# Kernel tuning notes

Measured on AMD Instinct MI355X. Metric: run time of the kernel, lower is better.

The kernel has to match this reference:

```python
import jax, jax.numpy as jnp
import numpy as np

STRIDE = 1
PADDING = 1

def setup_inputs() -> dict:
    key = jax.random.key(0)
    k1, k2 = jax.random.split(key)
    x = jax.random.normal(k1, (16, 64, 224, 224), dtype=jnp.float32)
    weight = jax.random.normal(k2, (64, 64, 3, 3), dtype=jnp.float32)
    return {"x": x, "weight": weight}

def reference(x, weight):
    # Module's per-tap shift-and-add loop is exactly cross-correlation conv2d:
    # weight indexed [out, in, kh, kw] with ZeroPad2d(padding) and given stride.
    return jax.lax.conv_general_dilated(
        x, weight,
        window_strides=(STRIDE, STRIDE),
        padding=((PADDING, PADDING), (PADDING, PADDING)),
        dimension_numbers=("NCHW", "OIHW", "NCHW"),
    )
```

## Files before the change

### kernel.cpp

```cpp
#include <hip/hip_runtime.h>


#define HH 224
#define WW 224
#define CHW (HH * WW)
#define PLANE 4352
#define NSLOT 18

typedef short bf16x8 __attribute__((ext_vector_type(8)));
typedef float f32x16 __attribute__((ext_vector_type(16)));

__device__ __forceinline__ unsigned short f2bf(float f) {
    union { float f; unsigned int u; } v; v.f = f;
    unsigned int u = v.u;
    return (unsigned short)((u + 0x7fffu + ((u >> 16) & 1u)) >> 16);
}

#define SGB  __builtin_amdgcn_sched_group_barrier
#define MFMA __builtin_amdgcn_mfma_f32_32x32x16_bf16

__device__ __forceinline__ void block_fence_lds() {
    asm volatile("s_waitcnt lgkmcnt(0)" ::: "memory");
    __builtin_amdgcn_s_barrier();
    __builtin_amdgcn_sched_barrier(0);
}

__global__ void wprep_kernel(const float* __restrict__ wgt, unsigned short* __restrict__ wb) {
    const int i = blockIdx.x * 256 + threadIdx.x;
    if (i >= 36864) return;
    const int j   = i & 7;
    const int oc  = (i >> 3) & 63;
    const int g   = (i >> 9) & 1;
    const int ks  = i >> 10;
    const int tap = ks >> 2;
    const int c   = (ks & 3) * 16 + g * 8 + j;
    wb[i] = f2bf(wgt[(oc * 64 + c) * 9 + tap]);
}

#define MMA_CQ(dw, cq, WFU) do {                                              \
    const int off_ = (((cq) * 32 + g16) ^ swz_);                              \
    const bf16x8 B0 = *(const bf16x8*)(ldsB + sl0 + wb_ + off_);              \
    const bf16x8 B1 = *(const bf16x8*)(ldsB + sl1 + wb_ + off_);              \
    const bf16x8 B2 = *(const bf16x8*)(ldsB + sl2 + wb_ + off_);              \
    const bf16x8 B3 = *(const bf16x8*)(ldsB + sl3 + wb_ + off_);              \
    const bf16x8 B4 = *(const bf16x8*)(ldsB + sl4 + wb_ + off_);              \
    const bf16x8 B5 = *(const bf16x8*)(ldsB + sl5 + wb_ + off_);              \
    a0 = MFMA(wfrag[(dw)*4 + (cq)], B0, a0, 0, 0, 0);                         \
    a1 = MFMA(wfrag[(dw)*4 + (cq)], B1, a1, 0, 0, 0);                         \
    a2 = MFMA(wfrag[(dw)*4 + (cq)], B2, a2, 0, 0, 0);                         \
    a3 = MFMA(wfrag[(dw)*4 + (cq)], B3, a3, 0, 0, 0);                         \
    a0 = MFMA(wfrag[12 + (dw)*4 + (cq)], B1, a0, 0, 0, 0);                    \
    a1 = MFMA(wfrag[12 + (dw)*4 + (cq)], B2, a1, 0, 0, 0);                    \
    a2 = MFMA(wfrag[12 + (dw)*4 + (cq)], B3, a2, 0, 0, 0);                    \
    a3 = MFMA(wfrag[12 + (dw)*4 + (cq)], B4, a3, 0, 0, 0);                    \
    a0 = MFMA(WFU, B2, a0, 0, 0, 0);                                          \
    a1 = MFMA(WFU, B3, a1, 0, 0, 0);                                          \
    a2 = MFMA(WFU, B4, a2, 0, 0, 0);                                          \
    a3 = MFMA(WFU, B5, a3, 0, 0, 0);                                          \
    SGB(0x100, 6, 0); SGB(0x008, 12, 0);                                      \
} while (0)

#define SECTION(dw, cqp, WFU0, WFU1, WFLD0, WFLD1, ldw, lcqp) do {            \
    WFLD0 = *(const bf16x8*)(wlane + ((6 + (ldw))*4 + 2*(lcqp)    ) * 1024);  \
    WFLD1 = *(const bf16x8*)(wlane + ((6 + (ldw))*4 + 2*(lcqp) + 1) * 1024);  \
    const int wl_  = s + (dw);                                                \
    const int swz_ = (wl_ & 7) << 4;                                          \
    const int wb_  = wl_ * 128;                                               \
    MMA_CQ(dw, 2*(cqp),     WFU0);                                            \
    MMA_CQ(dw, 2*(cqp) + 1, WFU1);                                            \
} while (0)

#define STI(k) do { if (st) {                                                 \
    const int r_ = h + 9 + (k);                                               \
    const bool ok_ = (r_ < HH);                                               \
    _Pragma("unroll")                                                         \
    for (int j = 0; j < 8; ++j) pv[j] = ok_ ? pxm[j*CHW + r_*WW] : 0.f;       \
    if (tid >= 240) {                                                         \
        const bool okh_ = ok_ && hokw;                                        \
        _Pragma("unroll")                                                     \
        for (int j = 0; j < 8; ++j) hv[j] = okh_ ? pxh[j*CHW + r_*WW] : 0.f;  \
    } } } while (0)

#define STW(k) do { if (st) {                                                 \
    int sw_ = slw + (k); if (sw_ >= NSLOT) sw_ -= NSLOT;                      \
    bf16x8 f_;                                                                \
    _Pragma("unroll")                                                         \
    for (int j = 0; j < 8; ++j) f_[j] = (short)f2bf(pv[j]);                   \
    *(bf16x8*)(ldsB + sw_ * PLANE + lom) = f_;                                \
    if (tid >= 240) {                                                         \
        bf16x8 fh_;                                                           \
        _Pragma("unroll")                                                     \
        for (int j = 0; j < 8; ++j) fh_[j] = (short)f2bf(hv[j]);              \
        *(bf16x8*)(ldsB + sw_ * PLANE + loh) = fh_;                           \
    } } } while (0)

__global__ __launch_bounds__(256, 2)
void conv3x3_mfma(const float* __restrict__ x, const unsigned short* __restrict__ wb,
                  float* __restrict__ out) {
    __shared__ __align__(16) unsigned short lds[NSLOT * 34 * 64];
    char* ldsB = (char*)lds;

    const int tid  = threadIdx.x;
    const int lane = tid & 63;
    const int wv   = tid >> 6;
    const int och  = wv & 1;
    const int rg4  = wv >> 1;
    const int s    = lane & 31;
    const int g    = lane >> 5;
    const int g16  = g * 16;

    const int bid = blockIdx.x;
    const int n   = bid / 28;
    const int rem = bid % 28;
    const int ws  = rem / 4;
    const int hc  = rem % 4;
    const int wbase = ws * 32;
    const int h0    = hc * 56;

    const unsigned short* wlane = wb + g * 512 + (och * 32 + s) * 8;
    bf16x8 wfrag[24];
#pragma unroll
    for (int ks = 0; ks < 24; ++ks)
        wfrag[ks] = *(const bf16x8*)(wlane + ks * 1024);
    bf16x8 wfA0 = *(const bf16x8*)(wlane + 24 * 1024);
    bf16x8 wfA1 = *(const bf16x8*)(wlane + 25 * 1024);
    bf16x8 wfB0 = {}, wfB1 = {};

    for (int p = tid; p < 10 * 272; p += 256) {
        const int rrel = p / 272;
        const int q  = p % 272;
        const int c8 = q / 34;
        const int wl = q % 34;
        const int r  = h0 - 1 + rrel;
        const int gw = wbase - 1 + wl;
        bf16x8 f = {};
        if (r >= 0 && r < HH && gw >= 0 && gw < WW) {
            const float* px = x + (n * 64 + c8 * 8) * CHW + r * WW + gw;
#pragma unroll
            for (int j = 0; j < 8; ++j) f[j] = (short)f2bf(px[j * CHW]);
        }
        *(bf16x8*)(ldsB + ((r + NSLOT) % NSLOT) * PLANE + wl * 128
                   + ((c8 * 16) ^ ((wl & 7) << 4))) = f;
    }

    const int c8m = tid >> 5;
    const int wlm = 1 + (tid & 31);
    const float* pxm = x + (n * 64 + c8m * 8) * CHW + (wbase + (tid & 31));
    const int lom = wlm * 128 + ((c8m * 16) ^ ((wlm & 7) << 4));
    const int c8h = lane & 7;
    const int wlh = ((lane >> 3) & 1) * 33;
    const int gwh = wbase - 1 + wlh;
    const bool hokw = (gwh >= 0 && gwh < WW);
    const float* pxh = x + (n * 64 + c8h * 8) * CHW + gwh;
    const int loh = wlh * 128 + ((c8h * 16) ^ ((wlh & 7) << 4));

    block_fence_lds();

#pragma unroll 1
    for (int it = 0; it < 7; ++it) {
        const int h  = h0 + 8 * it;
        const int hb = h + 4 * rg4;
        const bool st = (it < 6);
        const int slw = (h + 9) % NSLOT;

        int t_ = (hb - 1 + NSLOT) % NSLOT;
        const int sl0 = t_ * PLANE; t_ = (t_ + 1 == NSLOT) ? 0 : t_ + 1;
        const int sl1 = t_ * PLANE; t_ = (t_ + 1 == NSLOT) ? 0 : t_ + 1;
        const int sl2 = t_ * PLANE; t_ = (t_ + 1 == NSLOT) ? 0 : t_ + 1;
        const int sl3 = t_ * PLANE; t_ = (t_ + 1 == NSLOT) ? 0 : t_ + 1;
        const int sl4 = t_ * PLANE; t_ = (t_ + 1 == NSLOT) ? 0 : t_ + 1;
        const int sl5 = t_ * PLANE;

        float pv[8], hv[8];
        f32x16 a0 = {}, a1 = {}, a2 = {}, a3 = {};

        STI(0); SECTION(0, 0, wfA0, wfA1, wfB0, wfB1, 0, 1); STW(0);
        STI(1); SECTION(0, 1, wfB0, wfB1, wfA0, wfA1, 1, 0); STW(1);
        STI(2); SECTION(1, 0, wfA0, wfA1, wfB0, wfB1, 1, 1); STW(2);
        STI(3); SECTION(1, 1, wfB0, wfB1, wfA0, wfA1, 2, 0); STW(3);
        STI(4); SECTION(2, 0, wfA0, wfA1, wfB0, wfB1, 2, 1); STW(4);
        STI(5); SECTION(2, 1, wfB0, wfB1, wfA0, wfA1, 0, 0); STW(5);

        float* po = out + (n * 64 + och * 32 + 4 * g) * CHW + hb * WW + wbase + s;
        STI(6);
#pragma unroll
        for (int rg = 0; rg < 16; ++rg) {
            const int o_ = ((rg & 3) + 8 * (rg >> 2)) * CHW;
            po[o_]      = a0[rg];
            po[o_ + WW] = a1[rg];
        }
        STW(6); STI(7);
#pragma unroll
        for (int rg = 0; rg < 16; ++rg) {
            const int o_ = ((rg & 3) + 8 * (rg >> 2)) * CHW;
            po[o_ + 2 * WW] = a2[rg];
            po[o_ + 3 * WW] = a3[rg];
        }
        STW(7);

        block_fence_lds();
    }
}

extern "C" void kernel_launch(void* const* d_in, const int* in_sizes, int n_in,
                              void* d_out, int out_size, void* d_ws, size_t ws_size,
                              hipStream_t stream) {
    const float* x   = (const float*)d_in[0];
    const float* wgt = (const float*)d_in[1];
    float* out       = (float*)d_out;
    unsigned short* wbuf = (unsigned short*)d_ws;

    wprep_kernel<<<dim3(144), dim3(256), 0, stream>>>(wgt, wbuf);
    conv3x3_mfma<<<dim3(448), dim3(256), 0, stream>>>(x, wbuf, out);
}
```

Before: 177.5 us.

## Halve per-block row tile, shrink LDS ring, raise occupancy to three blocks

Each block now covers 28 rows instead of 56, with each wave computing 2 output rows instead of 4. The grid doubles to 896 blocks and the LDS ring shrinks from 18 to 10 slots. Only 12 weight fragments stay resident and the rest stream through a three-deep rotation, cutting VGPR and LDS use so that launch bounds can ask for 3 blocks per CU. The cost is a larger halo overhead per block (6 loaded rows for 4 computed) and fewer MFMAs per barrier, which may reduce reuse and latency hiding.

```diff
diff --git a/kernel.cpp b/kernel.cpp
--- a/kernel.cpp
+++ b/kernel.cpp
@@ -5,7 +5,7 @@
 #define WW 224
 #define CHW (HH * WW)
 #define PLANE 4352
-#define NSLOT 18
+#define NSLOT 10
 
 typedef short bf16x8 __attribute__((ext_vector_type(8)));
 typedef float f32x16 __attribute__((ext_vector_type(16)));
@@ -37,64 +37,49 @@
     wb[i] = f2bf(wgt[(oc * 64 + c) * 9 + tap]);
 }
 
-#define MMA_CQ(dw, cq, WFU) do {                                              \
-    const int off_ = (((cq) * 32 + g16) ^ swz_);                              \
-    const bf16x8 B0 = *(const bf16x8*)(ldsB + sl0 + wb_ + off_);              \
-    const bf16x8 B1 = *(const bf16x8*)(ldsB + sl1 + wb_ + off_);              \
-    const bf16x8 B2 = *(const bf16x8*)(ldsB + sl2 + wb_ + off_);              \
-    const bf16x8 B3 = *(const bf16x8*)(ldsB + sl3 + wb_ + off_);              \
-    const bf16x8 B4 = *(const bf16x8*)(ldsB + sl4 + wb_ + off_);              \
-    const bf16x8 B5 = *(const bf16x8*)(ldsB + sl5 + wb_ + off_);              \
-    a0 = MFMA(wfrag[(dw)*4 + (cq)], B0, a0, 0, 0, 0);                         \
-    a1 = MFMA(wfrag[(dw)*4 + (cq)], B1, a1, 0, 0, 0);                         \
-    a2 = MFMA(wfrag[(dw)*4 + (cq)], B2, a2, 0, 0, 0);                         \
-    a3 = MFMA(wfrag[(dw)*4 + (cq)], B3, a3, 0, 0, 0);                         \
-    a0 = MFMA(wfrag[12 + (dw)*4 + (cq)], B1, a0, 0, 0, 0);                    \
-    a1 = MFMA(wfrag[12 + (dw)*4 + (cq)], B2, a1, 0, 0, 0);                    \
-    a2 = MFMA(wfrag[12 + (dw)*4 + (cq)], B3, a2, 0, 0, 0);                    \
-    a3 = MFMA(wfrag[12 + (dw)*4 + (cq)], B4, a3, 0, 0, 0);                    \
-    a0 = MFMA(WFU, B2, a0, 0, 0, 0);                                          \
-    a1 = MFMA(WFU, B3, a1, 0, 0, 0);                                          \
-    a2 = MFMA(WFU, B4, a2, 0, 0, 0);                                          \
-    a3 = MFMA(WFU, B5, a3, 0, 0, 0);                                          \
-    SGB(0x100, 6, 0); SGB(0x008, 12, 0);                                      \
+#define STEP(j, U1_, U2_, L1_, L2_) do {                                      \
+    L1_ = *(const bf16x8*)(wlane + (12 + ((j) + 2) % 12) * 1024);             \
+    L2_ = *(const bf16x8*)(wlane + (24 + ((j) + 2) % 12) * 1024);             \
+    const int wl_  = s + ((j) >> 2);                                          \
+    const int off_ = wl_ * 128 + ((((j) & 3) * 32 + g16) ^ ((wl_ & 7) << 4)); \
+    const bf16x8 B0 = *(const bf16x8*)(ldsB + sl0 + off_);                    \
+    const bf16x8 B1 = *(const bf16x8*)(ldsB + sl1 + off_);                    \
+    const bf16x8 B2 = *(const bf16x8*)(ldsB + sl2 + off_);                    \
+    const bf16x8 B3 = *(const bf16x8*)(ldsB + sl3 + off_);                    \
+    a0 = MFMA(wfrag[(j)], B0, a0, 0, 0, 0);                                   \
+    a1 = MFMA(wfrag[(j)], B1, a1, 0, 0, 0);                                   \
+    a0 = MFMA(U1_, B1, a0, 0, 0, 0);                                          \
+    a1 = MFMA(U1_, B2, a1, 0, 0, 0);                                          \
+    a0 = MFMA(U2_, B2, a0, 0, 0, 0);                                          \
+    a1 = MFMA(U2_, B3, a1, 0, 0, 0);                                          \
+    SGB(0x100, 4, 0); SGB(0x008, 6, 0);                                       \
 } while (0)
 
-#define SECTION(dw, cqp, WFU0, WFU1, WFLD0, WFLD1, ldw, lcqp) do {            \
-    WFLD0 = *(const bf16x8*)(wlane + ((6 + (ldw))*4 + 2*(lcqp)    ) * 1024);  \
-    WFLD1 = *(const bf16x8*)(wlane + ((6 + (ldw))*4 + 2*(lcqp) + 1) * 1024);  \
-    const int wl_  = s + (dw);                                                \
-    const int swz_ = (wl_ & 7) << 4;                                          \
-    const int wb_  = wl_ * 128;                                               \
-    MMA_CQ(dw, 2*(cqp),     WFU0);                                            \
-    MMA_CQ(dw, 2*(cqp) + 1, WFU1);                                            \
-} while (0)
-
-#define STI(k) do { if (st) {                                                 \
-    const int r_ = h + 9 + (k);                                               \
+#define STI(k, PV) do { if (st) {                                             \
+    const int r_ = h + 5 + (k);                                               \
     const bool ok_ = (r_ < HH);                                               \
     _Pragma("unroll")                                                         \
-    for (int j = 0; j < 8; ++j) pv[j] = ok_ ? pxm[j*CHW + r_*WW] : 0.f;       \
-    if (tid >= 240) {                                                         \
+    for (int j = 0; j < 8; ++j) PV[j] = ok_ ? pxm[j*CHW + r_*WW] : 0.f;       \
+    if (tid >= 192 && hrow == (k)) {                                          \
         const bool okh_ = ok_ && hokw;                                        \
         _Pragma("unroll")                                                     \
         for (int j = 0; j < 8; ++j) hv[j] = okh_ ? pxh[j*CHW + r_*WW] : 0.f;  \
     } } } while (0)
 
-#define STW(k) do { if (st) {                                                 \
-    int sw_ = slw + (k); if (sw_ >= NSLOT) sw_ -= NSLOT;                      \
+#define STW(k, PV) do { if (st) {                                             \
+    const int sw_ = ((h + 5 + (k)) % NSLOT) * PLANE;                          \
     bf16x8 f_;                                                                \
     _Pragma("unroll")                                                         \
-    for (int j = 0; j < 8; ++j) f_[j] = (short)f2bf(pv[j]);                   \
-    *(bf16x8*)(ldsB + sw_ * PLANE + lom) = f_;                                \
-    if (tid >= 240) {                                                         \
+    for (int j = 0; j < 8; ++j) f_[j] = (short)f2bf(PV[j]);                   \
+    *(bf16x8*)(ldsB + sw_ + lom) = f_;                                        \
+    if (tid >= 192 && hrow == (k)) {                                          \
         bf16x8 fh_;                                                           \
         _Pragma("unroll")                                                     \
         for (int j = 0; j < 8; ++j) fh_[j] = (short)f2bf(hv[j]);              \
-        *(bf16x8*)(ldsB + sw_ * PLANE + loh) = fh_;                           \
+        *(bf16x8*)(ldsB + sw_ + loh) = fh_;                                   \
     } } } while (0)
 
-__global__ __launch_bounds__(256, 2)
+__global__ __launch_bounds__(256, 3)
 void conv3x3_mfma(const float* __restrict__ x, const unsigned short* __restrict__ wb,
                   float* __restrict__ out) {
     __shared__ __align__(16) unsigned short lds[NSLOT * 34 * 64];
@@ -104,29 +89,31 @@
     const int lane = tid & 63;
     const int wv   = tid >> 6;
     const int och  = wv & 1;
-    const int rg4  = wv >> 1;
+    const int rp   = wv >> 1;
     const int s    = lane & 31;
     const int g    = lane >> 5;
     const int g16  = g * 16;
 
     const int bid = blockIdx.x;
-    const int n   = bid / 28;
-    const int rem = bid % 28;
-    const int ws  = rem / 4;
-    const int hc  = rem % 4;
+    const int n   = bid / 56;
+    const int rem = bid % 56;
+    const int ws  = rem / 8;
+    const int hc  = rem % 8;
     const int wbase = ws * 32;
-    const int h0    = hc * 56;
+    const int h0    = hc * 28;
 
     const unsigned short* wlane = wb + g * 512 + (och * 32 + s) * 8;
-    bf16x8 wfrag[24];
+    bf16x8 wfrag[12];
 #pragma unroll
-    for (int ks = 0; ks < 24; ++ks)
+    for (int ks = 0; ks < 12; ++ks)
         wfrag[ks] = *(const bf16x8*)(wlane + ks * 1024);
-    bf16x8 wfA0 = *(const bf16x8*)(wlane + 24 * 1024);
-    bf16x8 wfA1 = *(const bf16x8*)(wlane + 25 * 1024);
-    bf16x8 wfB0 = {}, wfB1 = {};
-
-    for (int p = tid; p < 10 * 272; p += 256) {
+    bf16x8 Q0a = *(const bf16x8*)(wlane + 12 * 1024);
+    bf16x8 Q0b = *(const bf16x8*)(wlane + 24 * 1024);
+    bf16x8 Q1a = *(const bf16x8*)(wlane + 13 * 1024);
+    bf16x8 Q1b = *(const bf16x8*)(wlane + 25 * 1024);
+    bf16x8 Q2a, Q2b;
+
+    for (int p = tid; p < 6 * 272; p += 256) {
         const int rrel = p / 272;
         const int q  = p % 272;
         const int c8 = q / 34;
@@ -139,7 +126,7 @@
 #pragma unroll
             for (int j = 0; j < 8; ++j) f[j] = (short)f2bf(px[j * CHW]);
         }
-        *(bf16x8*)(ldsB + ((r + NSLOT) % NSLOT) * PLANE + wl * 128
+        *(bf16x8*)(ldsB + ((r + 2 * NSLOT) % NSLOT) * PLANE + wl * 128
                    + ((c8 * 16) ^ ((wl & 7) << 4))) = f;
     }
 
@@ -147,9 +134,10 @@
     const int wlm = 1 + (tid & 31);
     const float* pxm = x + (n * 64 + c8m * 8) * CHW + (wbase + (tid & 31));
     const int lom = wlm * 128 + ((c8m * 16) ^ ((wlm & 7) << 4));
-    const int c8h = lane & 7;
-    const int wlh = ((lane >> 3) & 1) * 33;
-    const int gwh = wbase - 1 + wlh;
+    const int hrow = (tid >> 4) & 3;
+    const int c8h  = tid & 7;
+    const int wlh  = ((tid >> 3) & 1) * 33;
+    const int gwh  = wbase - 1 + wlh;
     const bool hokw = (gwh >= 0 && gwh < WW);
     const float* pxh = x + (n * 64 + c8h * 8) * CHW + gwh;
     const int loh = wlh * 128 + ((c8h * 16) ^ ((wlh & 7) << 4));
@@ -158,45 +146,44 @@
 
 #pragma unroll 1
     for (int it = 0; it < 7; ++it) {
-        const int h  = h0 + 8 * it;
-        const int hb = h + 4 * rg4;
+        const int h  = h0 + 4 * it;
+        const int hb = h + 2 * rp;
         const bool st = (it < 6);
-        const int slw = (h + 9) % NSLOT;
-
-        int t_ = (hb - 1 + NSLOT) % NSLOT;
-        const int sl0 = t_ * PLANE; t_ = (t_ + 1 == NSLOT) ? 0 : t_ + 1;
-        const int sl1 = t_ * PLANE; t_ = (t_ + 1 == NSLOT) ? 0 : t_ + 1;
-        const int sl2 = t_ * PLANE; t_ = (t_ + 1 == NSLOT) ? 0 : t_ + 1;
-        const int sl3 = t_ * PLANE; t_ = (t_ + 1 == NSLOT) ? 0 : t_ + 1;
-        const int sl4 = t_ * PLANE; t_ = (t_ + 1 == NSLOT) ? 0 : t_ + 1;
-        const int sl5 = t_ * PLANE;
-
-        float pv[8], hv[8];
-        f32x16 a0 = {}, a1 = {}, a2 = {}, a3 = {};
-
-        STI(0); SECTION(0, 0, wfA0, wfA1, wfB0, wfB1, 0, 1); STW(0);
-        STI(1); SECTION(0, 1, wfB0, wfB1, wfA0, wfA1, 1, 0); STW(1);
-        STI(2); SECTION(1, 0, wfA0, wfA1, wfB0, wfB1, 1, 1); STW(2);
-        STI(3); SECTION(1, 1, wfB0, wfB1, wfA0, wfA1, 2, 0); STW(3);
-        STI(4); SECTION(2, 0, wfA0, wfA1, wfB0, wfB1, 2, 1); STW(4);
-        STI(5); SECTION(2, 1, wfB0, wfB1, wfA0, wfA1, 0, 0); STW(5);
+
+        const int sl0 = ((hb - 1 + 2 * NSLOT) % NSLOT) * PLANE;
+        const int sl1 = ((hb     + 2 * NSLOT) % NSLOT) * PLANE;
+        const int sl2 = ((hb + 1) % NSLOT) * PLANE;
+        const int sl3 = ((hb + 2) % NSLOT) * PLANE;
+
+        float pv0[8], pv1[8], hv[8];
+        f32x16 a0 = {}, a1 = {};
+
+        STI(0, pv0); STI(1, pv1);
+
+        STEP(0, Q0a, Q0b, Q2a, Q2b);
+        STEP(1, Q1a, Q1b, Q0a, Q0b);
+        STEP(2, Q2a, Q2b, Q1a, Q1b);
+        STW(0, pv0); STI(2, pv0);
+        STEP(3, Q0a, Q0b, Q2a, Q2b);
+        STEP(4, Q1a, Q1b, Q0a, Q0b);
+        STEP(5, Q2a, Q2b, Q1a, Q1b);
+        STW(1, pv1); STI(3, pv1);
+        STEP(6, Q0a, Q0b, Q2a, Q2b);
+        STEP(7, Q1a, Q1b, Q0a, Q0b);
+        STW(2, pv0);
+        STEP(8, Q2a, Q2b, Q1a, Q1b);
+        STEP(9, Q0a, Q0b, Q2a, Q2b);
+        STW(3, pv1);
+        STEP(10, Q1a, Q1b, Q0a, Q0b);
+        STEP(11, Q2a, Q2b, Q1a, Q1b);
 
         float* po = out + (n * 64 + och * 32 + 4 * g) * CHW + hb * WW + wbase + s;
-        STI(6);
 #pragma unroll
         for (int rg = 0; rg < 16; ++rg) {
             const int o_ = ((rg & 3) + 8 * (rg >> 2)) * CHW;
             po[o_]      = a0[rg];
             po[o_ + WW] = a1[rg];
         }
-        STW(6); STI(7);
-#pragma unroll
-        for (int rg = 0; rg < 16; ++rg) {
-            const int o_ = ((rg & 3) + 8 * (rg >> 2)) * CHW;
-            po[o_ + 2 * WW] = a2[rg];
-            po[o_ + 3 * WW] = a3[rg];
-        }
-        STW(7);
 
         block_fence_lds();
     }
@@ -211,5 +198,5 @@
     unsigned short* wbuf = (unsigned short*)d_ws;
 
     wprep_kernel<<<dim3(144), dim3(256), 0, stream>>>(wgt, wbuf);
-    conv3x3_mfma<<<dim3(448), dim3(256), 0, stream>>>(x, wbuf, out);
-}
+    conv3x3_mfma<<<dim3(16 * 7 * 8), dim3(256), 0, stream>>>(x, wbuf, out);
+}
```

Measured after the change: 233.1 us. 1.31x slower.

## Pre-transpose input to padded bf16 NHWC and stream rows via global_load_lds

Applied to the files above, without the earlier changes.

Adds a prep kernel that converts the fp32 NCHW input into a zero-padded, swizzled bf16 channels-last buffer in workspace. The main conv kernel then copies whole rows straight into LDS with global_load_lds, with no per-thread conversion or register staging, and drops the in-loop boundary checks. This removes the strided fp32 loads and bf16 conversion from the MFMA loop. The cost is an extra full pass over the input (reading about 200MB of fp32 and writing about 100MB of bf16) plus a second launch. The new path runs only if the workspace holds roughly 105MB; otherwise the old kernel is used.

```diff
diff --git a/kernel.cpp b/kernel.cpp
--- a/kernel.cpp
+++ b/kernel.cpp
@@ -1,4 +1,5 @@
 #include <hip/hip_runtime.h>
+#include <stdint.h>
 
 
 #define HH 224
@@ -6,9 +7,15 @@
 #define CHW (HH * WW)
 #define PLANE 4352
 #define NSLOT 18
+#define XT_ROWB 28928
+#define XT_NB   6537728
+#define WB_BYTES 73728
+#define WS_NEED (WB_BYTES + 16 * (size_t)XT_NB)
 
 typedef short bf16x8 __attribute__((ext_vector_type(8)));
 typedef float f32x16 __attribute__((ext_vector_type(16)));
+typedef __attribute__((address_space(1))) const char GCHAR;
+typedef __attribute__((address_space(3))) char LCHAR;
 
 __device__ __forceinline__ unsigned short f2bf(float f) {
     union { float f; unsigned int u; } v; v.f = f;
@@ -35,6 +42,41 @@
     const int tap = ks >> 2;
     const int c   = (ks & 3) * 16 + g * 8 + j;
     wb[i] = f2bf(wgt[(oc * 64 + c) * 9 + tap]);
+}
+
+__global__ __launch_bounds__(256)
+void xprep_kernel(const float* __restrict__ x, unsigned short* __restrict__ xt) {
+    __shared__ __align__(16) unsigned short tile[226 * 64];
+    const int tid = threadIdx.x;
+    const int b   = blockIdx.x;
+    const int n   = b / 226;
+    const int hp  = b % 226;
+    bf16x8* orow = (bf16x8*)((char*)xt + (size_t)(n * 226 + hp) * XT_ROWB);
+
+    if (hp == 0 || hp == 225) {
+        const bf16x8 z = {};
+        for (int i = tid; i < 1808; i += 256) orow[i] = z;
+        return;
+    }
+    if (tid < 64) { tile[tid] = 0; tile[225 * 64 + tid] = 0; }
+
+    const float* xr = x + (size_t)n * 64 * CHW + (size_t)(hp - 1) * WW;
+    for (int i = tid; i < 64 * 56; i += 256) {
+        const int c  = i / 56;
+        const int w4 = i % 56;
+        const float4 v = *(const float4*)(xr + (size_t)c * CHW + w4 * 4);
+        const int wp0 = w4 * 4 + 1;
+        const int cb  = c * 2;
+        *(unsigned short*)((char*)tile + (wp0    ) * 128 + (cb ^ ((((wp0    ) >> 2) & 7) << 4))) = f2bf(v.x);
+        *(unsigned short*)((char*)tile + (wp0 + 1) * 128 + (cb ^ ((((wp0 + 1) >> 2) & 7) << 4))) = f2bf(v.y);
+        *(unsigned short*)((char*)tile + (wp0 + 2) * 128 + (cb ^ ((((wp0 + 2) >> 2) & 7) << 4))) = f2bf(v.z);
+        *(unsigned short*)((char*)tile + (wp0 + 3) * 128 + (cb ^ ((((wp0 + 3) >> 2) & 7) << 4))) = f2bf(v.w);
+    }
+    __syncthreads();
+    for (int i = tid; i < 1808; i += 256) {
+        const int wp = i >> 3, k = i & 7;
+        orow[i] = ((const bf16x8*)tile)[wp * 8 + (k ^ ((wp >> 2) & 7))];
+    }
 }
 
 #define MMA_CQ(dw, cq, WFU) do {                                              \
@@ -70,6 +112,107 @@
     MMA_CQ(dw, 2*(cqp) + 1, WFU1);                                            \
 } while (0)
 
+#define GLOAD_ROW(r) do {                                                     \
+    const char* seg_ = xtn + (size_t)((r) + 1) * XT_ROWB;                     \
+    char* lp_ = ldsB + (((r) + NSLOT) % NSLOT) * PLANE;                       \
+    _Pragma("unroll")                                                         \
+    for (int p_ = 0; p_ < 4; ++p_)                                            \
+        __builtin_amdgcn_global_load_lds((GCHAR*)(seg_ + p_ * 1024 + lconst), \
+                                         (LCHAR*)(lp_ + p_ * 1024), 16, 0, 0);\
+    if (lane < 16)                                                            \
+        __builtin_amdgcn_global_load_lds((GCHAR*)(seg_ + 4096 + lconst),      \
+                                         (LCHAR*)(lp_ + 4096), 16, 0, 0);     \
+} while (0)
+
+__global__ __launch_bounds__(256, 2)
+void conv3x3_gl(const unsigned short* __restrict__ xt, const unsigned short* __restrict__ wb,
+                float* __restrict__ out) {
+    __shared__ __align__(16) unsigned short lds[NSLOT * 34 * 64];
+    char* ldsB = (char*)lds;
+
+    const int tid  = threadIdx.x;
+    const int lane = tid & 63;
+    const int wv   = tid >> 6;
+    const int och  = wv & 1;
+    const int rg4  = wv >> 1;
+    const int s    = lane & 31;
+    const int g    = lane >> 5;
+    const int g16  = g * 16;
+
+    const int bid = blockIdx.x;
+    const int n   = bid / 28;
+    const int rem = bid % 28;
+    const int ws  = rem / 4;
+    const int hc  = rem % 4;
+    const int wbase = ws * 32;
+    const int h0    = hc * 56;
+
+    const int lconst = ((lane >> 3) << 7) + (((lane & 7) ^ (lane >> 3)) << 4);
+    const char* xtn = (const char*)xt + (size_t)n * XT_NB + (size_t)wbase * 128;
+
+    const unsigned short* wlane = wb + g * 512 + (och * 32 + s) * 8;
+    bf16x8 wfrag[24];
+#pragma unroll
+    for (int ks = 0; ks < 24; ++ks)
+        wfrag[ks] = *(const bf16x8*)(wlane + ks * 1024);
+    bf16x8 wfA0 = *(const bf16x8*)(wlane + 24 * 1024);
+    bf16x8 wfA1 = *(const bf16x8*)(wlane + 25 * 1024);
+    bf16x8 wfB0 = {}, wfB1 = {};
+
+    for (int rr = 0; rr < 10; ++rr) {
+        const int r = h0 - 1 + rr;
+        const char* seg = xtn + (size_t)(r + 1) * XT_ROWB;
+        char* lp = ldsB + ((r + NSLOT) % NSLOT) * PLANE;
+        __builtin_amdgcn_global_load_lds((GCHAR*)(seg + wv * 1024 + lconst),
+                                         (LCHAR*)(lp + wv * 1024), 16, 0, 0);
+        if (wv == 0 && lane < 16)
+            __builtin_amdgcn_global_load_lds((GCHAR*)(seg + 4096 + lconst),
+                                             (LCHAR*)(lp + 4096), 16, 0, 0);
+    }
+    __syncthreads();
+
+#pragma unroll 1
+    for (int it = 0; it < 7; ++it) {
+        const int h  = h0 + 8 * it;
+        const int hb = h + 4 * rg4;
+
+        if (it < 6) {
+            const int r0 = h + 9 + 2 * wv;
+            GLOAD_ROW(r0);
+            GLOAD_ROW(r0 + 1);
+        }
+
+        int t_ = (hb - 1 + NSLOT) % NSLOT;
+        const int sl0 = t_ * PLANE; t_ = (t_ + 1 == NSLOT) ? 0 : t_ + 1;
+        const int sl1 = t_ * PLANE; t_ = (t_ + 1 == NSLOT) ? 0 : t_ + 1;
+        const int sl2 = t_ * PLANE; t_ = (t_ + 1 == NSLOT) ? 0 : t_ + 1;
+        const int sl3 = t_ * PLANE; t_ = (t_ + 1 == NSLOT) ? 0 : t_ + 1;
+        const int sl4 = t_ * PLANE; t_ = (t_ + 1 == NSLOT) ? 0 : t_ + 1;
+        const int sl5 = t_ * PLANE;
+
+        f32x16 a0 = {}, a1 = {}, a2 = {}, a3 = {};
+
+        SECTION(0, 0, wfA0, wfA1, wfB0, wfB1, 0, 1);
+        SECTION(0, 1, wfB0, wfB1, wfA0, wfA1, 1, 0);
+        SECTION(1, 0, wfA0, wfA1, wfB0, wfB1, 1, 1);
+        SECTION(1, 1, wfB0, wfB1, wfA0, wfA1, 2, 0);
+        SECTION(2, 0, wfA0, wfA1, wfB0, wfB1, 2, 1);
+        SECTION(2, 1, wfB0, wfB1, wfA0, wfA1, 0, 0);
+
+        float* po = out + (n * 64 + och * 32 + 4 * g) * CHW + hb * WW + wbase + s;
+#pragma unroll
+        for (int rg = 0; rg < 16; ++rg) {
+            const int o_ = ((rg & 3) + 8 * (rg >> 2)) * CHW;
+            po[o_]          = a0[rg];
+            po[o_ + WW]     = a1[rg];
+            po[o_ + 2 * WW] = a2[rg];
+            po[o_ + 3 * WW] = a3[rg];
+        }
+
+        __syncthreads();
+    }
+}
+
 #define STI(k) do { if (st) {                                                 \
     const int r_ = h + 9 + (k);                                               \
     const bool ok_ = (r_ < HH);                                               \
@@ -95,8 +238,8 @@
     } } } while (0)
 
 __global__ __launch_bounds__(256, 2)
-void conv3x3_mfma(const float* __restrict__ x, const unsigned short* __restrict__ wb,
-                  float* __restrict__ out) {
+void conv3x3_fb(const float* __restrict__ x, const unsigned short* __restrict__ wb,
+                float* __restrict__ out) {
     __shared__ __align__(16) unsigned short lds[NSLOT * 34 * 64];
     char* ldsB = (char*)lds;
 
@@ -211,5 +354,11 @@
     unsigned short* wbuf = (unsigned short*)d_ws;
 
     wprep_kernel<<<dim3(144), dim3(256), 0, stream>>>(wgt, wbuf);
-    conv3x3_mfma<<<dim3(448), dim3(256), 0, stream>>>(x, wbuf, out);
-}
+    if (ws_size >= WS_NEED) {
+        unsigned short* xt = (unsigned short*)((char*)d_ws + WB_BYTES);
+        xprep_kernel<<<dim3(16 * 226), dim3(256), 0, stream>>>(x, xt);
+        conv3x3_gl<<<dim3(448), dim3(256), 0, stream>>>(xt, wbuf, out);
+    } else {
+        conv3x3_fb<<<dim3(448), dim3(256), 0, stream>>>(x, wbuf, out);
+    }
+}
```

Result: faster. 161.6 us (-9.0%).
